# Kernel tuning notes

Hardware: AMD Instinct MI355X
Metric: run time of the kernel (lower is better)

Reference implementation:

```python
import jax, jax.numpy as jnp
import numpy as np
import math

N_HEADS = 8

def setup_inputs() -> dict:
    key = jax.random.key(0)
    qkv = jax.random.normal(key, (4, 1536, 2048), dtype=jnp.float32)
    return {"qkv": qkv}

def reference(qkv):
    bs, width, length = qkv.shape
    ch = width // (3 * N_HEADS)
    # reshape to [bs*n_heads, 3*ch, length] then split into q, k, v
    qkv_h = qkv.reshape(bs * N_HEADS, 3 * ch, length)
    q = qkv_h[:, :ch]
    k = qkv_h[:, ch:2 * ch]
    v = qkv_h[:, 2 * ch:]
    scale = 1.0 / math.sqrt(math.sqrt(ch))
    # scores: [B*H, T, S]
    weight = jnp.einsum('bct,bcs->bts', q * scale, k * scale)
    weight = jax.nn.softmax(weight.astype(jnp.float32), axis=-1).astype(weight.dtype)
    a = jnp.einsum('bts,bcs->bct', weight, v)  # [B*H, ch, T]
    return a.reshape(bs, N_HEADS * ch, length)
```

## Files before the change

### kernel.cpp

```cpp
#include <hip/hip_runtime.h>
#include <hip/hip_bf16.h>

typedef __attribute__((ext_vector_type(8))) short bf16x8;
typedef __attribute__((ext_vector_type(8))) unsigned short u16x8;
typedef __attribute__((ext_vector_type(4))) float f32x4;
typedef __attribute__((ext_vector_type(16))) float f32x16;

#define SEQ 2048
#define NBH 32
#define QSCALE 0.1803368801111204f

#if __has_builtin(__builtin_amdgcn_exp2f)
#define EXP2(x) __builtin_amdgcn_exp2f(x)
#else
#define EXP2(x) exp2f(x)
#endif

__device__ __forceinline__ unsigned short bfc(float f) {
  union { __hip_bfloat16 h; unsigned short u; } v;
  v.h = __float2bfloat16(f);
  return v.u;
}

__device__ __forceinline__ void gl_lds16(const void* g, void* l) {
  __builtin_amdgcn_global_load_lds((__attribute__((address_space(1))) void*)g,
                                   (__attribute__((address_space(3))) void*)l, 16, 0, 0);
}

__global__ __launch_bounds__(256)
void prep_kernel(const float* __restrict__ qkv, unsigned short* __restrict__ ws) {
  const int tid = threadIdx.x;
  const int b = blockIdx.x;
  if (b < 4096) {
    int gid = b * 256 + tid;
    int sec = gid >> 19;
    int r = gid & 524287;
    int bh = r >> 14;
    int rr = r & 16383;
    int cc = rr >> 11;
    int t = rr & 2047;
    const float* src = qkv + ((size_t)(bh >> 3) * 1536 + (bh & 7) * 192 + sec * 64 + cc * 8) * SEQ + t;
    const float scale = sec ? 1.0f : QSCALE;
    u16x8 o;
    #pragma unroll
    for (int e = 0; e < 8; ++e) o[e] = bfc(src[(size_t)e * SEQ] * scale);
    unsigned short* dst = ws + ((size_t)sec * NBH * SEQ + (size_t)bh * SEQ + t) * 64;
    *(u16x8*)(dst + ((cc ^ (t & 7)) * 8)) = o;
  } else {
    int cid = (b - 4096) * 256 + tid;
    int bh = cid >> 14;
    int rr = cid & 16383;
    int c = rr >> 8;
    int cc = rr & 255;
    int grp = cc >> 3, sub = cc & 7;
    const float* src = qkv + ((size_t)(bh >> 3) * 1536 + (bh & 7) * 192 + 128 + c) * SEQ + cc * 8;
    float4 a = *(const float4*)(src);
    float4 bv = *(const float4*)(src + 4);
    u16x8 o;
    o[0] = bfc(a.x); o[1] = bfc(a.y); o[2] = bfc(a.z); o[3] = bfc(a.w);
    o[4] = bfc(bv.x); o[5] = bfc(bv.y); o[6] = bfc(bv.z); o[7] = bfc(bv.w);
    unsigned short* dst = ws + (size_t)2 * NBH * SEQ * 64 +
                          ((size_t)bh * 64 + c) * SEQ + grp * 64 + ((sub ^ (c & 7)) * 8);
    *(u16x8*)dst = o;
  }
}

__global__ __launch_bounds__(512, 1)
void attn_main(const unsigned short* __restrict__ ws, float* __restrict__ out) {
  const int bid = blockIdx.x;
  const int bh = (bid & 7) + 8 * ((bid >> 3) >> 4);
  const int tile = (bid >> 3) & 15;
  const int t0 = tile * 128;

  const unsigned short* Qws = ws + ((size_t)bh * SEQ + t0) * 64;
  const unsigned short* Kws = ws + (size_t)NBH * SEQ * 64 + (size_t)bh * SEQ * 64;
  const unsigned short* Vws = ws + (size_t)2 * NBH * SEQ * 64 + (size_t)bh * 64 * SEQ;
  float* __restrict__ outb = out + (size_t)bh * 64 * SEQ;

  __shared__ __align__(16) char smem[65536];
  unsigned short* KtB = (unsigned short*)smem;
  unsigned short* VtB = (unsigned short*)(smem + 32768);

  const int tid = threadIdx.x;
  const int w = tid >> 6;
  const int ts = w & 1;
  const int sh = w >> 1;
  const int l = tid & 63;
  const int lw = l & 31;
  const int h = l >> 5;
  const int sw = lw & 7;

  bf16x8 qB[2][4];
  #pragma unroll
  for (int tsub = 0; tsub < 2; ++tsub) {
    const int rloc = ts * 64 + tsub * 32 + lw;
    #pragma unroll
    for (int kc = 0; kc < 4; ++kc)
      qB[tsub][kc] = *(const bf16x8*)&Qws[rloc * 64 + (((2 * kc + h) ^ sw) * 8)];
  }

  gl_lds16(Kws + (size_t)tid * 8, &KtB[tid * 8]);
  gl_lds16(Kws + (size_t)(tid + 512) * 8, &KtB[(tid + 512) * 8]);
  {
    int q = tid;       int c = q >> 4, g2 = (q >> 3) & 1, j = q & 7;
    gl_lds16(Vws + (size_t)c * SEQ + g2 * 64 + j * 8, &VtB[q * 8]);
    q = tid + 512;     c = q >> 4;     g2 = (q >> 3) & 1; j = q & 7;
    gl_lds16(Vws + (size_t)c * SEQ + g2 * 64 + j * 8, &VtB[q * 8]);
  }
  __syncthreads();

  f32x16 zero16;
  #pragma unroll
  for (int i = 0; i < 16; ++i) zero16[i] = 0.f;
  bf16x8 onesB;
  #pragma unroll
  for (int i = 0; i < 8; ++i) onesB[i] = (short)0x3F80;

  f32x16 accO[2][2];
  f32x16 psum[2];
  accO[0][0] = zero16; accO[0][1] = zero16;
  accO[1][0] = zero16; accO[1][1] = zero16;
  psum[0] = zero16; psum[1] = zero16;

  int cur = 0;
  #pragma unroll 1
  for (int it = 0; it < SEQ / 128; ++it) {
    {
      const int s1 = (it + 1) & 15;
      const unsigned short* kn = Kws + (size_t)s1 * 8192;
      unsigned short* kd = KtB + (cur ^ 1) * 8192;
      gl_lds16(kn + (size_t)tid * 8, &kd[tid * 8]);
      gl_lds16(kn + (size_t)(tid + 512) * 8, &kd[(tid + 512) * 8]);
      unsigned short* vd = VtB + (cur ^ 1) * 8192;
      int q = tid;     int c = q >> 4, g2 = (q >> 3) & 1, j = q & 7;
      gl_lds16(Vws + (size_t)c * SEQ + (2 * s1 + g2) * 64 + j * 8, &vd[q * 8]);
      q = tid + 512;   c = q >> 4;     g2 = (q >> 3) & 1; j = q & 7;
      gl_lds16(Vws + (size_t)c * SEQ + (2 * s1 + g2) * 64 + j * 8, &vd[q * 8]);
    }

    const unsigned short* kb = KtB + cur * 8192;
    const unsigned short* vb = VtB + cur * 8192;

    f32x16 accS[2];
    #pragma unroll
    for (int kc = 0; kc < 4; ++kc) {
      bf16x8 ka = *(const bf16x8*)&kb[(sh * 32 + lw) * 64 + (((2 * kc + h) ^ sw) * 8)];
      #pragma unroll
      for (int tsub = 0; tsub < 2; ++tsub)
        accS[tsub] = __builtin_amdgcn_mfma_f32_32x32x16_bf16(
            ka, qB[tsub][kc], kc ? accS[tsub] : zero16, 0, 0, 0);
    }

    #pragma unroll
    for (int tsub = 0; tsub < 2; ++tsub)
      #pragma unroll
      for (int r = 0; r < 16; ++r) accS[tsub][r] = EXP2(accS[tsub][r]);

    bf16x8 pA[2][2];
    #pragma unroll
    for (int tsub = 0; tsub < 2; ++tsub) {
      unsigned int pk[8];
      #pragma unroll
      for (int wd = 0; wd < 8; ++wd)
        asm("v_cvt_pk_bf16_f32 %0, %1, %2"
            : "=v"(pk[wd]) : "v"(accS[tsub][2 * wd]), "v"(accS[tsub][2 * wd + 1]));
      #pragma unroll
      for (int a = 0; a < 2; ++a) {
        unsigned int x0 = pk[4 * a + 0], y0 = pk[4 * a + 2];
        unsigned int x1 = pk[4 * a + 1], y1 = pk[4 * a + 3];
        asm("v_permlane32_swap_b32 %0, %1" : "+v"(x0), "+v"(y0));
        asm("v_permlane32_swap_b32 %0, %1" : "+v"(x1), "+v"(y1));
        union { unsigned int u[4]; bf16x8 v; } uu;
        uu.u[0] = x0; uu.u[1] = x1; uu.u[2] = y0; uu.u[3] = y1;
        pA[tsub][a] = uu.v;
      }
    }

    #pragma unroll
    for (int tsub = 0; tsub < 2; ++tsub)
      #pragma unroll
      for (int ks = 0; ks < 2; ++ks)
        psum[tsub] = __builtin_amdgcn_mfma_f32_32x32x16_bf16(pA[tsub][ks], onesB, psum[tsub], 0, 0, 0);

    #pragma unroll
    for (int ch = 0; ch < 2; ++ch) {
      #pragma unroll
      for (int ks = 0; ks < 2; ++ks) {
        bf16x8 vB = *(const bf16x8*)&vb[(32 * ch + lw) * 128 + (sh >> 1) * 64 +
                                        (((((sh & 1) * 4) + 2 * ks + h) ^ sw) * 8)];
        #pragma unroll
        for (int tsub = 0; tsub < 2; ++tsub)
          accO[tsub][ch] = __builtin_amdgcn_mfma_f32_32x32x16_bf16(pA[tsub][ks], vB, accO[tsub][ch], 0, 0, 0);
      }
    }

    __syncthreads();
    cur ^= 1;
  }

  float* red = (float*)smem;
  #pragma unroll
  for (int ch = 0; ch < 2; ++ch) {
    __syncthreads();
    if (sh != 0) {
      #pragma unroll
      for (int tsub = 0; tsub < 2; ++tsub)
        #pragma unroll
        for (int r = 0; r < 16; ++r)
          red[((((sh - 1) * 2 + ts) * 2 + tsub) * 16 + r) * 64 + l] = accO[tsub][ch][r];
    }
    __syncthreads();
    if (sh == 0) {
      #pragma unroll
      for (int tsub = 0; tsub < 2; ++tsub)
        #pragma unroll
        for (int r = 0; r < 16; ++r)
          #pragma unroll
          for (int p = 0; p < 3; ++p)
            accO[tsub][ch][r] += red[(((p * 2 + ts) * 2 + tsub) * 16 + r) * 64 + l];
    }
  }
  __syncthreads();
  if (sh != 0) {
    #pragma unroll
    for (int tsub = 0; tsub < 2; ++tsub)
      #pragma unroll
      for (int r = 0; r < 16; ++r)
        red[((((sh - 1) * 2 + ts) * 2 + tsub) * 16 + r) * 64 + l] = psum[tsub][r];
  }
  __syncthreads();
  if (sh == 0) {
    #pragma unroll
    for (int tsub = 0; tsub < 2; ++tsub) {
      float linv[16];
      #pragma unroll
      for (int r = 0; r < 16; ++r) {
        float pt = psum[tsub][r];
        #pragma unroll
        for (int p = 0; p < 3; ++p)
          pt += red[(((p * 2 + ts) * 2 + tsub) * 16 + r) * 64 + l];
        linv[r] = 1.0f / pt;
      }
      #pragma unroll
      for (int ch = 0; ch < 2; ++ch) {
        #pragma unroll
        for (int r = 0; r < 16; ++r) {
          const int tg = t0 + ts * 64 + tsub * 32 + (r & 3) + 8 * (r >> 2) + 4 * h;
          outb[(size_t)(32 * ch + lw) * SEQ + tg] = accO[tsub][ch][r] * linv[r];
        }
      }
    }
  }
}

#define PAD 72
#define BTF 128
__device__ __forceinline__ unsigned short f2bf(float f) {
  union { float f; unsigned u; } v; v.f = f;
  return (unsigned short)((v.u + 0x7fffu + ((v.u >> 16) & 1u)) >> 16);
}

__global__ __launch_bounds__(512, 4)
void qkv_attn_fallback(const float* __restrict__ qkv, float* __restrict__ out) {
  const int bid = blockIdx.x;
  const int xcd = bid & 7;
  const int slot = bid >> 3;
  const int bh = xcd + 8 * (slot >> 4);
  const int tile = slot & 15;
  const int t0 = tile * BTF;

  const float* __restrict__ base = qkv + (size_t)((bh >> 3) * 1536 + (bh & 7) * 192) * SEQ;
  const float* __restrict__ qg = base;
  const float* __restrict__ kg = base + 64 * SEQ;
  const float* __restrict__ vg = base + 128 * SEQ;
  float* __restrict__ outb = out + (size_t)bh * 64 * SEQ;

  __shared__ __align__(16) unsigned short Qt[BTF * PAD];
  __shared__ __align__(16) unsigned short Kt[64 * PAD];
  __shared__ __align__(16) unsigned short Vt[64 * PAD];
  __shared__ __align__(16) unsigned short Pl[BTF * PAD];

  const int tid = threadIdx.x;
  const int w = tid >> 6;
  const int l = tid & 63;
  const int lr = l & 15;
  const int g = l >> 4;

  {
    const int cb = tid >> 5, tb = tid & 31;
    const int c0 = cb * 4, tt0 = tb * 4;
    const float* p = qg + c0 * SEQ + t0 + tt0;
    float4 r0 = *(const float4*)(p);
    float4 r1 = *(const float4*)(p + SEQ);
    float4 r2 = *(const float4*)(p + 2 * SEQ);
    float4 r3 = *(const float4*)(p + 3 * SEQ);
    const float s = 0.125f;
    ushort4 w0 = { f2bf(r0.x*s), f2bf(r1.x*s), f2bf(r2.x*s), f2bf(r3.x*s) };
    ushort4 w1 = { f2bf(r0.y*s), f2bf(r1.y*s), f2bf(r2.y*s), f2bf(r3.y*s) };
    ushort4 w2 = { f2bf(r0.z*s), f2bf(r1.z*s), f2bf(r2.z*s), f2bf(r3.z*s) };
    ushort4 w3 = { f2bf(r0.w*s), f2bf(r1.w*s), f2bf(r2.w*s), f2bf(r3.w*s) };
    *(ushort4*)&Qt[(tt0 + 0) * PAD + c0] = w0;
    *(ushort4*)&Qt[(tt0 + 1) * PAD + c0] = w1;
    *(ushort4*)&Qt[(tt0 + 2) * PAD + c0] = w2;
    *(ushort4*)&Qt[(tt0 + 3) * PAD + c0] = w3;
  }
  __syncthreads();

  bf16x8 qB0 = *(const bf16x8*)&Qt[(w * 16 + lr) * PAD + g * 8];
  bf16x8 qB1 = *(const bf16x8*)&Qt[(w * 16 + lr) * PAD + g * 8 + 32];

  f32x4 pv[4];
  #pragma unroll
  for (int i = 0; i < 4; ++i) pv[i] = (f32x4){0.f, 0.f, 0.f, 0.f};
  float mrun = -1e30f;
  float lsum = 0.f;

  for (int s0 = 0; s0 < SEQ; s0 += 64) {
    __syncthreads();
    {
      const int cb = tid >> 4, sb = tid & 15;
      const int c0 = cb * 2, sl = sb * 4;
      const float* p0 = kg + c0 * SEQ + s0 + sl;
      float4 a0 = *(const float4*)(p0);
      float4 a1 = *(const float4*)(p0 + SEQ);
      ushort2 y0 = { f2bf(a0.x), f2bf(a1.x) };
      ushort2 y1 = { f2bf(a0.y), f2bf(a1.y) };
      ushort2 y2 = { f2bf(a0.z), f2bf(a1.z) };
      ushort2 y3 = { f2bf(a0.w), f2bf(a1.w) };
      *(ushort2*)&Kt[(sl + 0) * PAD + c0] = y0;
      *(ushort2*)&Kt[(sl + 1) * PAD + c0] = y1;
      *(ushort2*)&Kt[(sl + 2) * PAD + c0] = y2;
      *(ushort2*)&Kt[(sl + 3) * PAD + c0] = y3;
    }
    {
      const int c = tid >> 3;
      const int sq = (tid & 7) * 8;
      const float* p0 = vg + c * SEQ + s0 + sq;
      float4 b0 = *(const float4*)(p0);
      float4 b1 = *(const float4*)(p0 + 4);
      ushort4 z0 = { f2bf(b0.x), f2bf(b0.y), f2bf(b0.z), f2bf(b0.w) };
      ushort4 z1 = { f2bf(b1.x), f2bf(b1.y), f2bf(b1.z), f2bf(b1.w) };
      *(ushort4*)&Vt[c * PAD + sq] = z0;
      *(ushort4*)&Vt[c * PAD + sq + 4] = z1;
    }
    __syncthreads();

    f32x4 acc[4];
    #pragma unroll
    for (int i = 0; i < 4; ++i) acc[i] = (f32x4){0.f, 0.f, 0.f, 0.f};
    #pragma unroll
    for (int ch = 0; ch < 2; ++ch) {
      bf16x8 qb = ch ? qB1 : qB0;
      #pragma unroll
      for (int sub = 0; sub < 4; ++sub) {
        bf16x8 ka = *(const bf16x8*)&Kt[(sub * 16 + lr) * PAD + g * 8 + 32 * ch];
        acc[sub] = __builtin_amdgcn_mfma_f32_16x16x32_bf16(ka, qb, acc[sub], 0, 0, 0);
      }
    }

    float pmax = -1e30f;
    #pragma unroll
    for (int sub = 0; sub < 4; ++sub)
      #pragma unroll
      for (int r = 0; r < 4; ++r) pmax = fmaxf(pmax, acc[sub][r]);
    pmax = fmaxf(pmax, __shfl_xor(pmax, 16));
    pmax = fmaxf(pmax, __shfl_xor(pmax, 32));
    const float mnew = fmaxf(mrun, pmax);
    const float alpha = __expf(mrun - mnew);
    float rsum = 0.f;
    #pragma unroll
    for (int sub = 0; sub < 4; ++sub) {
      #pragma unroll
      for (int r = 0; r < 4; ++r) {
        float p = __expf(acc[sub][r] - mnew);
        acc[sub][r] = p;
        rsum += p;
      }
    }
    rsum += __shfl_xor(rsum, 16);
    rsum += __shfl_xor(rsum, 32);
    lsum = lsum * alpha + rsum;
    mrun = mnew;

    #pragma unroll
    for (int sub = 0; sub < 4; ++sub) {
      ushort4 pw = { f2bf(acc[sub][0]), f2bf(acc[sub][1]), f2bf(acc[sub][2]), f2bf(acc[sub][3]) };
      *(ushort4*)&Pl[(w * 16 + lr) * PAD + sub * 16 + g * 4] = pw;
    }

    {
      const int sbase = (l & 48) + g * 4;
      #pragma unroll
      for (int r = 0; r < 4; ++r) {
        float ar = __shfl(alpha, sbase + r, 64);
        #pragma unroll
        for (int cs = 0; cs < 4; ++cs) pv[cs][r] *= ar;
      }
    }

    bf16x8 pA0 = *(const bf16x8*)&Pl[(w * 16 + lr) * PAD + g * 8];
    bf16x8 pA1 = *(const bf16x8*)&Pl[(w * 16 + lr) * PAD + g * 8 + 32];
    #pragma unroll
    for (int cs = 0; cs < 4; ++cs) {
      bf16x8 v0 = *(const bf16x8*)&Vt[(cs * 16 + lr) * PAD + g * 8];
      bf16x8 v1 = *(const bf16x8*)&Vt[(cs * 16 + lr) * PAD + g * 8 + 32];
      pv[cs] = __builtin_amdgcn_mfma_f32_16x16x32_bf16(pA0, v0, pv[cs], 0, 0, 0);
      pv[cs] = __builtin_amdgcn_mfma_f32_16x16x32_bf16(pA1, v1, pv[cs], 0, 0, 0);
    }
  }

  {
    const int sbase = (l & 48) + g * 4;
    float linv[4];
    #pragma unroll
    for (int r = 0; r < 4; ++r) linv[r] = 1.0f / __shfl(lsum, sbase + r, 64);
    #pragma unroll
    for (int cs = 0; cs < 4; ++cs) {
      #pragma unroll
      for (int r = 0; r < 4; ++r) {
        outb[(cs * 16 + lr) * SEQ + t0 + w * 16 + g * 4 + r] = pv[cs][r] * linv[r];
      }
    }
  }
}

extern "C" void kernel_launch(void* const* d_in, const int* in_sizes, int n_in,
                              void* d_out, int out_size, void* d_ws, size_t ws_size,
                              hipStream_t stream) {
  const float* qkv = (const float*)d_in[0];
  float* out = (float*)d_out;
  const size_t need = (size_t)3 * NBH * SEQ * 64 * sizeof(unsigned short);
  if (ws_size >= need) {
    unsigned short* ws = (unsigned short*)d_ws;
    prep_kernel<<<dim3(6144), dim3(256), 0, stream>>>(qkv, ws);
    attn_main<<<dim3(512), dim3(512), 0, stream>>>(ws, out);
  } else {
    qkv_attn_fallback<<<dim3(512), dim3(512), 0, stream>>>(qkv, out);
  }
}
```

Baseline: 65.49 us.

## Halve attention block to 256 threads with 64-key tiles and two blocks per CU

```diff
diff --git a/kernel.cpp b/kernel.cpp
--- a/kernel.cpp
+++ b/kernel.cpp
@@ -65,7 +65,7 @@
   }
 }
 
-__global__ __launch_bounds__(512, 1)
+__global__ __launch_bounds__(256, 2)
 void attn_main(const unsigned short* __restrict__ ws, float* __restrict__ out) {
   const int bid = blockIdx.x;
   const int bh = (bid & 7) + 8 * ((bid >> 3) >> 4);
@@ -77,9 +77,9 @@
   const unsigned short* Vws = ws + (size_t)2 * NBH * SEQ * 64 + (size_t)bh * 64 * SEQ;
   float* __restrict__ outb = out + (size_t)bh * 64 * SEQ;
 
-  __shared__ __align__(16) char smem[65536];
+  __shared__ __align__(16) char smem[32768];
   unsigned short* KtB = (unsigned short*)smem;
-  unsigned short* VtB = (unsigned short*)(smem + 32768);
+  unsigned short* VtB = (unsigned short*)(smem + 16384);
 
   const int tid = threadIdx.x;
   const int w = tid >> 6;
@@ -99,14 +99,13 @@
       qB[tsub][kc] = *(const bf16x8*)&Qws[rloc * 64 + (((2 * kc + h) ^ sw) * 8)];
   }
 
+  const int vc = tid >> 3, vj = tid & 7;
+  const int vc2 = vc + 32;
+
   gl_lds16(Kws + (size_t)tid * 8, &KtB[tid * 8]);
-  gl_lds16(Kws + (size_t)(tid + 512) * 8, &KtB[(tid + 512) * 8]);
-  {
-    int q = tid;       int c = q >> 4, g2 = (q >> 3) & 1, j = q & 7;
-    gl_lds16(Vws + (size_t)c * SEQ + g2 * 64 + j * 8, &VtB[q * 8]);
-    q = tid + 512;     c = q >> 4;     g2 = (q >> 3) & 1; j = q & 7;
-    gl_lds16(Vws + (size_t)c * SEQ + g2 * 64 + j * 8, &VtB[q * 8]);
-  }
+  gl_lds16(Kws + (size_t)(tid + 256) * 8, &KtB[(tid + 256) * 8]);
+  gl_lds16(Vws + (size_t)vc * SEQ + vj * 8, &VtB[tid * 8]);
+  gl_lds16(Vws + (size_t)vc2 * SEQ + vj * 8, &VtB[(tid + 256) * 8]);
   __syncthreads();
 
   f32x16 zero16;
@@ -124,22 +123,20 @@
 
   int cur = 0;
   #pragma unroll 1
-  for (int it = 0; it < SEQ / 128; ++it) {
+  for (int it = 0; it < SEQ / 64; ++it) {
     {
-      const int s1 = (it + 1) & 15;
-      const unsigned short* kn = Kws + (size_t)s1 * 8192;
-      unsigned short* kd = KtB + (cur ^ 1) * 8192;
+      const int s1 = (it + 1) & 31;
+      const unsigned short* kn = Kws + (size_t)s1 * 4096;
+      unsigned short* kd = KtB + (cur ^ 1) * 4096;
       gl_lds16(kn + (size_t)tid * 8, &kd[tid * 8]);
-      gl_lds16(kn + (size_t)(tid + 512) * 8, &kd[(tid + 512) * 8]);
-      unsigned short* vd = VtB + (cur ^ 1) * 8192;
-      int q = tid;     int c = q >> 4, g2 = (q >> 3) & 1, j = q & 7;
-      gl_lds16(Vws + (size_t)c * SEQ + (2 * s1 + g2) * 64 + j * 8, &vd[q * 8]);
-      q = tid + 512;   c = q >> 4;     g2 = (q >> 3) & 1; j = q & 7;
-      gl_lds16(Vws + (size_t)c * SEQ + (2 * s1 + g2) * 64 + j * 8, &vd[q * 8]);
-    }
-
-    const unsigned short* kb = KtB + cur * 8192;
-    const unsigned short* vb = VtB + cur * 8192;
+      gl_lds16(kn + (size_t)(tid + 256) * 8, &kd[(tid + 256) * 8]);
+      unsigned short* vd = VtB + (cur ^ 1) * 4096;
+      gl_lds16(Vws + (size_t)vc * SEQ + s1 * 64 + vj * 8, &vd[tid * 8]);
+      gl_lds16(Vws + (size_t)vc2 * SEQ + s1 * 64 + vj * 8, &vd[(tid + 256) * 8]);
+    }
+
+    const unsigned short* kb = KtB + cur * 4096;
+    const unsigned short* vb = VtB + cur * 4096;
 
     f32x16 accS[2];
     #pragma unroll
@@ -186,8 +183,7 @@
     for (int ch = 0; ch < 2; ++ch) {
       #pragma unroll
       for (int ks = 0; ks < 2; ++ks) {
-        bf16x8 vB = *(const bf16x8*)&vb[(32 * ch + lw) * 128 + (sh >> 1) * 64 +
-                                        (((((sh & 1) * 4) + 2 * ks + h) ^ sw) * 8)];
+        bf16x8 vB = *(const bf16x8*)&vb[(32 * ch + lw) * 64 + (((sh * 4 + 2 * ks + h) ^ sw) * 8)];
         #pragma unroll
         for (int tsub = 0; tsub < 2; ++tsub)
           accO[tsub][ch] = __builtin_amdgcn_mfma_f32_32x32x16_bf16(pA[tsub][ks], vB, accO[tsub][ch], 0, 0, 0);
@@ -199,34 +195,32 @@
   }
 
   float* red = (float*)smem;
-  #pragma unroll
-  for (int ch = 0; ch < 2; ++ch) {
-    __syncthreads();
-    if (sh != 0) {
-      #pragma unroll
-      for (int tsub = 0; tsub < 2; ++tsub)
+  if (sh == 1) {
+    #pragma unroll
+    for (int tsub = 0; tsub < 2; ++tsub)
+      #pragma unroll
+      for (int ch = 0; ch < 2; ++ch)
         #pragma unroll
         for (int r = 0; r < 16; ++r)
-          red[((((sh - 1) * 2 + ts) * 2 + tsub) * 16 + r) * 64 + l] = accO[tsub][ch][r];
-    }
-    __syncthreads();
-    if (sh == 0) {
-      #pragma unroll
-      for (int tsub = 0; tsub < 2; ++tsub)
+          red[(((ts * 2 + tsub) * 2 + ch) * 16 + r) * 64 + l] = accO[tsub][ch][r];
+  }
+  __syncthreads();
+  if (sh == 0) {
+    #pragma unroll
+    for (int tsub = 0; tsub < 2; ++tsub)
+      #pragma unroll
+      for (int ch = 0; ch < 2; ++ch)
         #pragma unroll
         for (int r = 0; r < 16; ++r)
-          #pragma unroll
-          for (int p = 0; p < 3; ++p)
-            accO[tsub][ch][r] += red[(((p * 2 + ts) * 2 + tsub) * 16 + r) * 64 + l];
-    }
+          accO[tsub][ch][r] += red[(((ts * 2 + tsub) * 2 + ch) * 16 + r) * 64 + l];
   }
   __syncthreads();
-  if (sh != 0) {
+  if (sh == 1) {
     #pragma unroll
     for (int tsub = 0; tsub < 2; ++tsub)
       #pragma unroll
       for (int r = 0; r < 16; ++r)
-        red[((((sh - 1) * 2 + ts) * 2 + tsub) * 16 + r) * 64 + l] = psum[tsub][r];
+        red[((ts * 2 + tsub) * 16 + r) * 64 + l] = psum[tsub][r];
   }
   __syncthreads();
   if (sh == 0) {
@@ -234,13 +228,8 @@
     for (int tsub = 0; tsub < 2; ++tsub) {
       float linv[16];
       #pragma unroll
-      for (int r = 0; r < 16; ++r) {
-        float pt = psum[tsub][r];
-        #pragma unroll
-        for (int p = 0; p < 3; ++p)
-          pt += red[(((p * 2 + ts) * 2 + tsub) * 16 + r) * 64 + l];
-        linv[r] = 1.0f / pt;
-      }
+      for (int r = 0; r < 16; ++r)
+        linv[r] = 1.0f / (psum[tsub][r] + red[((ts * 2 + tsub) * 16 + r) * 64 + l]);
       #pragma unroll
       for (int ch = 0; ch < 2; ++ch) {
         #pragma unroll
@@ -433,7 +422,7 @@
   if (ws_size >= need) {
     unsigned short* ws = (unsigned short*)d_ws;
     prep_kernel<<<dim3(6144), dim3(256), 0, stream>>>(qkv, ws);
-    attn_main<<<dim3(512), dim3(512), 0, stream>>>(ws, out);
+    attn_main<<<dim3(512), dim3(256), 0, stream>>>(ws, out);
   } else {
     qkv_attn_fallback<<<dim3(512), dim3(512), 0, stream>>>(qkv, out);
   }
```

New measurement: 61.12 us. 6.7% less time.
